# Optimization experiments

Measured on AMD Instinct MI355X. Metric: run time of the kernel, lower is better.

The kernel has to match this reference:

```python
import jax, jax.numpy as jnp
import numpy as np

B, L, D = 4, 1024, 256
HD = 16                 # head_dim
H = D // HD             # num heads = 16
DI = 2 * D              # mamba d_inner (expand=2) = 512
S = 64                  # d_state
KC = 4                  # d_conv
DTR = max(1, D // 16)   # dt_rank = 16
SCALES = (1, 2, 4, 8)


def _lin_interp(x, L_out):
    # F.interpolate(mode='linear', align_corners=False) on (B, L_in, D)
    L_in = x.shape[1]
    pos = (jnp.arange(L_out, dtype=x.dtype) + 0.5) * (L_in / L_out) - 0.5
    pos = jnp.clip(pos, 0.0, L_in - 1)
    lo = jnp.floor(pos).astype(jnp.int32)
    hi = jnp.minimum(lo + 1, L_in - 1)
    w = (pos - lo.astype(x.dtype))[None, :, None]
    return x[:, lo] * (1.0 - w) + x[:, hi] * w


def setup_inputs() -> dict:
    key = jax.random.key(0)
    ks = jax.random.split(key, 24)
    sc = 0.02
    inp = {
        "x": jax.random.normal(ks[0], (B, L, D), jnp.float32),
        "ln_g": jnp.ones((D,), jnp.float32),
        "ln_b": jnp.zeros((D,), jnp.float32),
        # MultiScaleQuery: 4 per-scale projections + fuse
        "mq_w": sc * jax.random.normal(ks[1], (4, D, D), jnp.float32),
        "mq_b": sc * jax.random.normal(ks[2], (4, D), jnp.float32),
        "fuse_w": sc * jax.random.normal(ks[3], (D, 4 * D), jnp.float32),
        "fuse_b": sc * jax.random.normal(ks[4], (D,), jnp.float32),
        # Mamba params
        "in_proj_w": sc * jax.random.normal(ks[5], (2 * DI, D), jnp.float32),
        "conv_w": 0.2 * jax.random.normal(ks[6], (DI, KC), jnp.float32),
        "conv_b": sc * jax.random.normal(ks[7], (DI,), jnp.float32),
        "x_proj_w": sc * jax.random.normal(ks[8], (DTR + 2 * S, DI), jnp.float32),
        "dt_w": sc * jax.random.normal(ks[9], (DI, DTR), jnp.float32),
        "dt_b": jnp.full((DI,), -4.0, jnp.float32),  # softplus -> small dt
        "A_log": jnp.log(jnp.tile(jnp.arange(1, S + 1, dtype=jnp.float32), (DI, 1))),
        "D_ssm": jnp.ones((DI,), jnp.float32),
        "out_w": sc * jax.random.normal(ks[10], (D, DI), jnp.float32),
        # StructuredSSD (q comes from MultiScaleQuery override; q_proj unused)
        "k_w": sc * jax.random.normal(ks[11], (D, D), jnp.float32),
        "k_b": sc * jax.random.normal(ks[12], (D,), jnp.float32),
        "v_w": sc * jax.random.normal(ks[13], (D, D), jnp.float32),
        "v_b": sc * jax.random.normal(ks[14], (D,), jnp.float32),
        "o_w": sc * jax.random.normal(ks[15], (D, D), jnp.float32),
        "o_b": sc * jax.random.normal(ks[16], (D,), jnp.float32),
        "log_tau": jnp.full((H,), np.log(16.0), jnp.float32),
        # Gate
        "gate_w": sc * jax.random.normal(ks[17], (D, 2 * D), jnp.float32),
        "gate_b": sc * jax.random.normal(ks[18], (D,), jnp.float32),
    }
    return inp


def reference(x, ln_g, ln_b, mq_w, mq_b, fuse_w, fuse_b,
              in_proj_w, conv_w, conv_b, x_proj_w, dt_w, dt_b,
              A_log, D_ssm, out_w,
              k_w, k_b, v_w, v_b, o_w, o_b, log_tau,
              gate_w, gate_b):
    Bsz, Lq, Dm = x.shape

    # ---- LayerNorm ----
    mu = x.mean(-1, keepdims=True)
    var = ((x - mu) ** 2).mean(-1, keepdims=True)
    xn = (x - mu) / jnp.sqrt(var + 1e-5) * ln_g + ln_b

    # ---- MultiScaleQuery ----
    qs = []
    for i, s in enumerate(SCALES):
        if s <= 1:
            q = xn @ mq_w[i].T + mq_b[i]
        else:
            xd = xn.reshape(Bsz, Lq // s, s, Dm).mean(2)   # avg_pool1d(k=s, stride=s)
            qd = xd @ mq_w[i].T + mq_b[i]
            q = _lin_interp(qd, Lq)
        qs.append(q)
    q = jnp.concatenate(qs, -1) @ fuse_w.T + fuse_b        # (B, L, D)

    # ---- Mamba (selective scan) ----
    xz = xn @ in_proj_w.T                                  # (B, L, 2*DI)
    xm, z = jnp.split(xz, 2, axis=-1)
    xp = jnp.pad(xm, ((0, 0), (KC - 1, 0), (0, 0)))        # causal depthwise conv
    xc = sum(xp[:, kk:kk + Lq, :] * conv_w[:, kk] for kk in range(KC)) + conv_b
    xc = jax.nn.silu(xc)                                   # (B, L, DI)
    dbc = xc @ x_proj_w.T                                  # (B, L, DTR+2S)
    dt_in, Bm, Cm = jnp.split(dbc, [DTR, DTR + S], axis=-1)
    dt = jax.nn.softplus(dt_in @ dt_w.T + dt_b)            # (B, L, DI)
    A = -jnp.exp(A_log)                                    # (DI, S)

    def step(h, inp):
        xt, dtt, Bt, Ct = inp                              # (B,DI) (B,DI) (B,S) (B,S)
        dA = jnp.exp(dtt[:, :, None] * A)                  # (B, DI, S)
        h = dA * h + (dtt * xt)[:, :, None] * Bt[:, None, :]
        y = jnp.einsum('bds,bs->bd', h, Ct)
        return h, y

    h0 = jnp.zeros((Bsz, DI, S), x.dtype)
    _, ys = jax.lax.scan(step, h0, (xc.transpose(1, 0, 2), dt.transpose(1, 0, 2),
                                    Bm.transpose(1, 0, 2), Cm.transpose(1, 0, 2)))
    y = ys.transpose(1, 0, 2) + xc * D_ssm                 # (B, L, DI)
    y = y * jax.nn.silu(z)
    ssm_out = y @ out_w.T                                  # (B, L, D)

    # ---- StructuredSSD (decay-masked attention, q override) ----
    k = xn @ k_w.T + k_b
    v = xn @ v_w.T + v_b
    hds = lambda t: t.reshape(Bsz, Lq, H, HD).transpose(0, 2, 1, 3)
    qh, kh, vh = hds(q), hds(k), hds(v)                    # (B, H, L, hd)
    scale = 1.0 / np.sqrt(HD)
    scores = jnp.einsum('bhqd,bhkd->bhqk', qh, kh) * scale
    idx = jnp.arange(Lq)
    dist = jnp.maximum(idx[:, None] - idx[None, :], 0).astype(x.dtype)
    tau = jnp.exp(log_tau)[:, None, None]                  # (H,1,1)
    mask = jnp.exp(-dist / tau)                            # (H, L, L); ==1 above diag
    scores = scores * mask
    denom = jnp.maximum(mask.sum(-1, keepdims=True), 1e-6)
    scores = scores / denom                                # broadcast over batch
    attn = jnp.einsum('bhqk,bhkd->bhqd', scores, vh)
    attn = attn.transpose(0, 2, 1, 3).reshape(Bsz, Lq, Dm)
    ssd_out = attn @ o_w.T + o_b

    # ---- Sigmoid gate fusion + residual ----
    gate = jax.nn.sigmoid(jnp.concatenate([ssm_out, ssd_out], -1) @ gate_w.T + gate_b)
    fused = gate * ssm_out + (1.0 - gate) * ssd_out
    return x + fused
```

## Files before the change

### kernel.cpp

```cpp
#include <hip/hip_runtime.h>
#include <math.h>

#define Bsz 4
#define Lseq 1024
#define Dm 256
#define Hh 16
#define HDm 16
#define DIm 512
#define Ssz 64
#define DTRm 16
#define NCH (Bsz * DIm)
#define CHK 64
#define NCHK (Lseq / CHK)
#define CHA 16
#define NCA (Lseq / CHA)
#define LOG2E 1.44269504088896f

typedef __attribute__((ext_vector_type(8))) short s8v;
typedef __attribute__((ext_vector_type(4))) short s4v;
typedef __attribute__((ext_vector_type(4))) float f4v;
typedef unsigned short u16;

static __device__ __forceinline__ float wave_sum(float v) {
    #pragma unroll
    for (int m = 32; m >= 1; m >>= 1) v += __shfl_xor(v, m, 64);
    return v;
}

static __device__ __forceinline__ float bcast(float v, int l) {
    return __uint_as_float(__builtin_amdgcn_readlane(__float_as_uint(v), l));
}

static __device__ __forceinline__ short f2bf(float f) {
    unsigned int u = __float_as_uint(f);
    u = (u + 0x7fffu + ((u >> 16) & 1u)) >> 16;
    return (short)u;
}

static __device__ __forceinline__ float bf2f(u16 u) {
    return __uint_as_float(((unsigned int)u) << 16);
}

static __device__ __forceinline__ s8v pack8(float4 a, float4 b) {
    s8v v;
    v[0] = f2bf(a.x); v[1] = f2bf(a.y); v[2] = f2bf(a.z); v[3] = f2bf(a.w);
    v[4] = f2bf(b.x); v[5] = f2bf(b.y); v[6] = f2bf(b.z); v[7] = f2bf(b.w);
    return v;
}

static __device__ __forceinline__ s4v pack4(float4 a) {
    s4v v;
    v[0] = f2bf(a.x); v[1] = f2bf(a.y); v[2] = f2bf(a.z); v[3] = f2bf(a.w);
    return v;
}

static __device__ __forceinline__ void mfma_core(const u16* __restrict__ A, int lda,
                                                 const u16* __restrict__ W, int ldw,
                                                 int m0, int n0, int K,
                                                 u16 (*As)[40], u16 (*Ws)[40],
                                                 f4v acc[2][2], int tid) {
    int wave = tid >> 6, lane = tid & 63;
    int quad = lane >> 4, r = lane & 15;
    int mo = (wave >> 1) * 32, no = (wave & 1) * 32;
    for (int k0 = 0; k0 < K; k0 += 32) {
        {
            int m = tid >> 2, kk = (tid & 3) * 8;
            *(s8v*)&As[m][kk] = *(const s8v*)(A + (size_t)(m0 + m) * lda + k0 + kk);
        }
        {
            int n = tid >> 2, kk = (tid & 3) * 8;
            *(s8v*)&Ws[n][kk] = *(const s8v*)(W + (size_t)(n0 + n) * ldw + k0 + kk);
        }
        __syncthreads();
        s8v af[2], bf[2];
        #pragma unroll
        for (int i = 0; i < 2; i++) af[i] = *(const s8v*)&As[mo + i * 16 + r][quad * 8];
        #pragma unroll
        for (int j = 0; j < 2; j++) bf[j] = *(const s8v*)&Ws[no + j * 16 + r][quad * 8];
        #pragma unroll
        for (int i = 0; i < 2; i++)
            #pragma unroll
            for (int j = 0; j < 2; j++)
                acc[i][j] = __builtin_amdgcn_mfma_f32_16x16x32_bf16(af[i], bf[j], acc[i][j], 0, 0, 0);
        __syncthreads();
    }
}

#define WB_INPJ 0
#define WB_K    262144
#define WB_V    327680
#define WB_MQ   393216
#define WB_FUSE 655360
#define WB_XP   917504
#define WB_OUT  991232
#define WB_O    1122304
#define WB_GATE 1187840
#define WB_OUTT 1318912
#define WB_WDT  1449984
#define WB_W1P  1712128

__global__ __launch_bounds__(256) void ln_pool(const float* __restrict__ x,
                                               const float* __restrict__ g,
                                               const float* __restrict__ bb,
                                               u16* __restrict__ xnb, u16* __restrict__ xd2b,
                                               u16* __restrict__ xd4b, u16* __restrict__ xd8b,
                                               const float* __restrict__ in_proj_w,
                                               const float* __restrict__ k_w,
                                               const float* __restrict__ v_w,
                                               const float* __restrict__ mq_w,
                                               const float* __restrict__ fuse_w,
                                               const float* __restrict__ x_proj_w,
                                               const float* __restrict__ out_w,
                                               const float* __restrict__ o_w,
                                               const float* __restrict__ gate_w,
                                               const float* __restrict__ dt_w,
                                               u16* __restrict__ wbf) {
    int bx = blockIdx.x;
    int tid = threadIdx.x;
    if (bx < 512) {
        __shared__ float p2[4][256];
        int wid = tid >> 6, lane = tid & 63;
        int gr0 = bx * 8;
        int b = gr0 >> 10, t0 = gr0 & 1023;
        float4 g4 = *(const float4*)(g + lane * 4);
        float4 b4 = *(const float4*)(bb + lane * 4);
        float4 res[2];
        #pragma unroll
        for (int rr = 0; rr < 2; rr++) {
            int row = gr0 + wid * 2 + rr;
            float4 xv = *(const float4*)(x + (size_t)row * 256 + lane * 4);
            float s = wave_sum(xv.x + xv.y + xv.z + xv.w);
            float mean = s * (1.0f / 256.0f);
            float d0 = xv.x - mean, d1 = xv.y - mean, d2 = xv.z - mean, d3 = xv.w - mean;
            float s2 = wave_sum(d0 * d0 + d1 * d1 + d2 * d2 + d3 * d3);
            float inv = rsqrtf(s2 * (1.0f / 256.0f) + 1e-5f);
            float4 r;
            r.x = d0 * inv * g4.x + b4.x; r.y = d1 * inv * g4.y + b4.y;
            r.z = d2 * inv * g4.z + b4.z; r.w = d3 * inv * g4.w + b4.w;
            *(s4v*)(xnb + (size_t)row * 256 + lane * 4) = pack4(r);
            res[rr] = r;
        }
        float4 a2;
        a2.x = 0.5f * (res[0].x + res[1].x); a2.y = 0.5f * (res[0].y + res[1].y);
        a2.z = 0.5f * (res[0].z + res[1].z); a2.w = 0.5f * (res[0].w + res[1].w);
        *(s4v*)(xd2b + (size_t)(b * 512 + (t0 >> 1) + wid) * 256 + lane * 4) = pack4(a2);
        *(float4*)&p2[wid][lane * 4] = a2;
        __syncthreads();
        if (wid < 2) {
            float4 u = *(const float4*)&p2[2 * wid][lane * 4];
            float4 w = *(const float4*)&p2[2 * wid + 1][lane * 4];
            float4 m;
            m.x = 0.5f * (u.x + w.x); m.y = 0.5f * (u.y + w.y);
            m.z = 0.5f * (u.z + w.z); m.w = 0.5f * (u.w + w.w);
            *(s4v*)(xd4b + (size_t)(b * 256 + (t0 >> 2) + wid) * 256 + lane * 4) = pack4(m);
        } else if (wid == 2) {
            float4 q0 = *(const float4*)&p2[0][lane * 4];
            float4 q1 = *(const float4*)&p2[1][lane * 4];
            float4 q2 = *(const float4*)&p2[2][lane * 4];
            float4 q3 = *(const float4*)&p2[3][lane * 4];
            float4 m;
            m.x = 0.25f * ((q0.x + q1.x) + (q2.x + q3.x));
            m.y = 0.25f * ((q0.y + q1.y) + (q2.y + q3.y));
            m.z = 0.25f * ((q0.z + q1.z) + (q2.z + q3.z));
            m.w = 0.25f * ((q0.w + q1.w) + (q2.w + q3.w));
            *(s4v*)(xd8b + (size_t)(b * 128 + (t0 >> 3)) * 256 + lane * 4) = pack4(m);
        }
    } else if (bx < 1156) {
        int l = bx - 512;
        const float* src; u16* dst; int base;
        if (l < 128)      { src = in_proj_w; dst = wbf + WB_INPJ; base = l; }
        else if (l < 160) { src = k_w;      dst = wbf + WB_K;    base = l - 128; }
        else if (l < 192) { src = v_w;      dst = wbf + WB_V;    base = l - 160; }
        else if (l < 320) { src = mq_w;     dst = wbf + WB_MQ;   base = l - 192; }
        else if (l < 448) { src = fuse_w;   dst = wbf + WB_FUSE; base = l - 320; }
        else if (l < 484) { src = x_proj_w; dst = wbf + WB_XP;   base = l - 448; }
        else if (l < 548) { src = out_w;    dst = wbf + WB_OUT;  base = l - 484; }
        else if (l < 580) { src = o_w;      dst = wbf + WB_O;    base = l - 548; }
        else              { src = gate_w;   dst = wbf + WB_GATE; base = l - 580; }
        int idx = base * 2048 + tid * 8;
        const float* sp = src + idx;
        *(s8v*)(dst + idx) = pack8(*(const float4*)sp, *(const float4*)(sp + 4));
    } else if (bx < 1412) {
        int l = bx - 1156;
        int gid = l * 1024 + tid * 4;
        int n = gid >> 9, d0 = gid & 511;
        float4 acc = {0.f, 0.f, 0.f, 0.f};
        #pragma unroll
        for (int k = 0; k < 16; k++) {
            float wv = dt_w[n * 16 + k];
            float4 xp = *(const float4*)(x_proj_w + (size_t)k * 512 + d0);
            acc.x = fmaf(wv, xp.x, acc.x); acc.y = fmaf(wv, xp.y, acc.y);
            acc.z = fmaf(wv, xp.z, acc.z); acc.w = fmaf(wv, xp.w, acc.w);
        }
        *(s4v*)(wbf + WB_WDT + (size_t)n * 512 + d0) = pack4(acc);
    } else {
        int l = bx - 1412;
        int gid = l * 2048 + tid * 8;
        int k = gid >> 9, d0 = gid & 511;
        float4 a0 = *(const float4*)(out_w + (size_t)k * 512 + d0);
        float4 a1 = *(const float4*)(out_w + (size_t)k * 512 + d0 + 4);
        float vv[8] = {a0.x, a0.y, a0.z, a0.w, a1.x, a1.y, a1.z, a1.w};
        #pragma unroll
        for (int i = 0; i < 8; i++)
            wbf[WB_OUTT + (size_t)(d0 + i) * 256 + k] = (u16)f2bf(vv[i]);
    }
}

__global__ __launch_bounds__(256) void proj8(const u16* __restrict__ xnb,
                                             const u16* __restrict__ xd2b,
                                             const u16* __restrict__ xd4b,
                                             const u16* __restrict__ xd8b,
                                             u16* __restrict__ wbf,
                                             const float* __restrict__ k_b,
                                             const float* __restrict__ v_b,
                                             const float* __restrict__ mq_b,
                                             u16* __restrict__ xmb, float* __restrict__ zT,
                                             float* __restrict__ kmat, float* __restrict__ vmat,
                                             u16* __restrict__ q0b, u16* __restrict__ qd2b,
                                             u16* __restrict__ qd4b, u16* __restrict__ qd8b) {
    __shared__ u16 As[64][40];
    __shared__ u16 Ws[64][40];
    int bx = blockIdx.x;
    int tid = threadIdx.x;
    const u16* A; const u16* W; const float* bias;
    float* Cf = nullptr; u16* Cb = nullptr;
    int lda, ldw, ldc, K = 256, n0, m0;
    if (bx < 512) {
        A = xnb; lda = 256; W = wbf + WB_INPJ; ldw = 256; bias = nullptr; Cb = xmb; ldc = DIm;
        n0 = (bx & 7) * 64; m0 = (bx >> 3) * 64;
    } else if (bx < 1024) {
        int l = bx - 512;
        A = wbf + WB_INPJ + 131072; lda = 256; W = xnb; ldw = 256; bias = nullptr;
        Cf = zT; ldc = 4096;
        m0 = (l >> 6) * 64; n0 = (l & 63) * 64;
    } else if (bx < 1280) {
        int l = bx - 1024;
        A = xnb; lda = 256; W = wbf + WB_K; ldw = 256; bias = k_b; Cf = kmat; ldc = Dm;
        n0 = (l & 3) * 64; m0 = (l >> 2) * 64;
    } else if (bx < 1536) {
        int l = bx - 1280;
        A = xnb; lda = 256; W = wbf + WB_V; ldw = 256; bias = v_b; Cf = vmat; ldc = Dm;
        n0 = (l & 3) * 64; m0 = (l >> 2) * 64;
    } else if (bx < 1792) {
        int l = bx - 1536;
        A = xnb; lda = 256; W = wbf + WB_MQ; ldw = 256; bias = mq_b; Cb = q0b; ldc = Dm;
        n0 = (l & 3) * 64; m0 = (l >> 2) * 64;
    } else if (bx < 1920) {
        int l = bx - 1792;
        A = xd2b; lda = 256; W = wbf + WB_MQ + 65536; ldw = 256; bias = mq_b + 256; Cb = qd2b; ldc = Dm;
        n0 = (l & 3) * 64; m0 = (l >> 2) * 64;
    } else if (bx < 1984) {
        int l = bx - 1920;
        A = xd4b; lda = 256; W = wbf + WB_MQ + 131072; ldw = 256; bias = mq_b + 512; Cb = qd4b; ldc = Dm;
        n0 = (l & 3) * 64; m0 = (l >> 2) * 64;
    } else {
        if (bx < 2016) {
            int l = bx - 1984;
            A = xd8b; lda = 256; W = wbf + WB_MQ + 196608; ldw = 256; bias = mq_b + 768; Cb = qd8b; ldc = Dm;
            n0 = (l & 3) * 64; m0 = (l >> 2) * 64;
        } else {
            int l = bx - 2016;
            A = wbf + WB_GATE; lda = 512; W = wbf + WB_OUTT; ldw = 256; bias = nullptr;
            Cb = wbf + WB_W1P; ldc = 512;
            m0 = (l >> 3) * 64; n0 = (l & 7) * 64;
        }
    }
    f4v acc[2][2];
    #pragma unroll
    for (int i = 0; i < 2; i++)
        #pragma unroll
        for (int j = 0; j < 2; j++) acc[i][j] = (f4v){0.f, 0.f, 0.f, 0.f};
    mfma_core(A, lda, W, ldw, m0, n0, K, As, Ws, acc, tid);
    int wave = tid >> 6, lane = tid & 63;
    int quad = lane >> 4, r = lane & 15;
    int mo = (wave >> 1) * 32, no = (wave & 1) * 32;
    #pragma unroll
    for (int i = 0; i < 2; i++)
        #pragma unroll
        for (int j = 0; j < 2; j++)
            #pragma unroll
            for (int reg = 0; reg < 4; reg++) {
                int m = m0 + mo + i * 16 + quad * 4 + reg;
                int n = n0 + no + j * 16 + r;
                float v = acc[i][j][reg];
                if (bias) v += bias[n];
                if (Cb) Cb[(size_t)m * ldc + n] = (u16)f2bf(v);
                else Cf[(size_t)m * ldc + n] = v;
            }
}

__global__ __launch_bounds__(256) void mid2(const u16* __restrict__ q0b,
                                            const u16* __restrict__ qd2b,
                                            const u16* __restrict__ qd4b,
                                            const u16* __restrict__ qd8b,
                                            const u16* __restrict__ w_fuse,
                                            const float* __restrict__ fuse_b,
                                            float* __restrict__ qbuf,
                                            const u16* __restrict__ xmb,
                                            const float* __restrict__ cw,
                                            const float* __restrict__ cb,
                                            u16* __restrict__ xcb, float* __restrict__ xcT) {
    __shared__ __align__(16) char smem[16640];
    int bx = blockIdx.x;
    int tid = threadIdx.x;
    if (bx < 256) {
        u16 (*As)[40] = (u16(*)[40])smem;
        u16 (*Ws)[40] = (u16(*)[40])(smem + 5120);
        int wave = tid >> 6, lane = tid & 63;
        int quad = lane >> 4, r = lane & 15;
        int n0 = (bx & 3) * 64, m0 = (bx >> 2) * 64;
        int mo = (wave >> 1) * 32, no = (wave & 1) * 32;
        f4v acc[2][2];
        #pragma unroll
        for (int i = 0; i < 2; i++)
            #pragma unroll
            for (int j = 0; j < 2; j++) acc[i][j] = (f4v){0.f, 0.f, 0.f, 0.f};
        for (int k0 = 0; k0 < 1024; k0 += 32) {
            {
                int m = tid >> 2, kk = (tid & 3) * 8;
                int kg = k0 + kk;
                int seg = kg >> 8, dcol = kg & 255;
                int mg = m0 + m;
                s8v pv;
                if (seg == 0) {
                    pv = *(const s8v*)(q0b + (size_t)mg * 256 + dcol);
                } else {
                    int t = mg & 1023, b = mg >> 10;
                    int Lin = 512 >> (seg - 1);
                    const u16* qd = (seg == 1) ? qd2b : (seg == 2) ? qd4b : qd8b;
                    float pos = (t + 0.5f) * ((float)Lin / 1024.0f) - 0.5f;
                    pos = fminf(fmaxf(pos, 0.0f), (float)(Lin - 1));
                    int lo = (int)floorf(pos);
                    int hi = min(lo + 1, Lin - 1);
                    float w = pos - (float)lo;
                    s8v lv = *(const s8v*)(qd + ((size_t)(b * Lin + lo)) * 256 + dcol);
                    s8v hv = *(const s8v*)(qd + ((size_t)(b * Lin + hi)) * 256 + dcol);
                    #pragma unroll
                    for (int i = 0; i < 8; i++) {
                        float lf = bf2f((u16)lv[i]), hf = bf2f((u16)hv[i]);
                        pv[i] = f2bf(lf + w * (hf - lf));
                    }
                }
                *(s8v*)&As[m][kk] = pv;
            }
            {
                int n = tid >> 2, kk = (tid & 3) * 8;
                *(s8v*)&Ws[n][kk] = *(const s8v*)(w_fuse + (size_t)(n0 + n) * 1024 + k0 + kk);
            }
            __syncthreads();
            s8v af[2], bf[2];
            #pragma unroll
            for (int i = 0; i < 2; i++) af[i] = *(const s8v*)&As[mo + i * 16 + r][quad * 8];
            #pragma unroll
            for (int j = 0; j < 2; j++) bf[j] = *(const s8v*)&Ws[no + j * 16 + r][quad * 8];
            #pragma unroll
            for (int i = 0; i < 2; i++)
                #pragma unroll
                for (int j = 0; j < 2; j++)
                    acc[i][j] = __builtin_amdgcn_mfma_f32_16x16x32_bf16(af[i], bf[j], acc[i][j], 0, 0, 0);
            __syncthreads();
        }
        #pragma unroll
        for (int i = 0; i < 2; i++)
            #pragma unroll
            for (int j = 0; j < 2; j++)
                #pragma unroll
                for (int reg = 0; reg < 4; reg++) {
                    int m = m0 + mo + i * 16 + quad * 4 + reg;
                    int n = n0 + no + j * 16 + r;
                    qbuf[(size_t)m * 256 + n] = acc[i][j][reg] + fuse_b[n];
                }
    } else {
        float (*tile)[65] = (float(*)[65])smem;
        int blk = bx - 256;
        int cblk = blk & 7;
        int tblk = (blk >> 3) & 15;
        int b = blk >> 7;
        int c0 = cblk * 64, t0 = tblk * 64;
        int cc = tid & 63;
        int tw = tid >> 6;
        int c = c0 + cc;
        float w0 = cw[c * 4 + 0], w1 = cw[c * 4 + 1], w2 = cw[c * 4 + 2], w3 = cw[c * 4 + 3];
        float bias = cb[c];
        #pragma unroll 4
        for (int i = 0; i < 16; i++) {
            int tl = tw * 16 + i;
            int t = t0 + tl;
            const u16* base = xmb + ((size_t)(b * Lseq + t)) * DIm + c;
            float acc = bias + bf2f(base[0]) * w3;
            if (t >= 3) {
                acc += bf2f(base[-3 * DIm]) * w0 + bf2f(base[-2 * DIm]) * w1 + bf2f(base[-1 * DIm]) * w2;
            } else {
                if (t >= 1) acc += bf2f(base[-1 * DIm]) * w2;
                if (t >= 2) acc += bf2f(base[-2 * DIm]) * w1;
            }
            float r = acc / (1.0f + __expf(-acc));
            xcb[((size_t)(b * Lseq + t)) * DIm + c] = (u16)f2bf(r);
            tile[tl][cc] = r;
        }
        __syncthreads();
        int tcol = tid & 63;
        int crow0 = tid >> 6;
        #pragma unroll 4
        for (int j = 0; j < 16; j++) {
            int crow = crow0 * 16 + j;
            xcT[((size_t)(c0 + crow)) * (Bsz * Lseq) + b * Lseq + t0 + tcol] = tile[tcol][crow];
        }
    }
}

__global__ __launch_bounds__(256) void xproj_ap1(const u16* __restrict__ xcb,
                                                 const u16* __restrict__ wbf,
                                                 float* __restrict__ dbc2,
                                                 const float* __restrict__ dt_b,
                                                 float* __restrict__ dtmT,
                                                 const float* __restrict__ kmat,
                                                 const float* __restrict__ vmat,
                                                 const float* __restrict__ log_tau,
                                                 float* __restrict__ loc) {
    __shared__ __align__(16) char smem[10240];
    int bx = blockIdx.x;
    int tid = threadIdx.x;
    int wid = tid >> 6, lane = tid & 63;
    if (bx < 640) {
        u16 (*As)[40] = (u16(*)[40])smem;
        u16 (*Ws)[40] = (u16(*)[40])(smem + 5120);
        const u16* A; const u16* W;
        int lda, ldw, K, m0, n0, mode;
        if (bx < 128) {
            A = xcb; lda = 512; W = wbf + WB_XP + 16 * 512; ldw = 512; K = 512;
            n0 = (bx & 1) * 64; m0 = (bx >> 1) * 64; mode = 0;
        } else {
            int l = bx - 128;
            A = wbf + WB_WDT; lda = 512; W = xcb; ldw = 512; K = 512;
            m0 = (l >> 6) * 64; n0 = (l & 63) * 64; mode = 1;
        }
        f4v acc[2][2];
        #pragma unroll
        for (int i = 0; i < 2; i++)
            #pragma unroll
            for (int j = 0; j < 2; j++) acc[i][j] = (f4v){0.f, 0.f, 0.f, 0.f};
        mfma_core(A, lda, W, ldw, m0, n0, K, As, Ws, acc, tid);
        int quad = lane >> 4, r = lane & 15;
        int mo = (wid >> 1) * 32, no = (wid & 1) * 32;
        #pragma unroll
        for (int i = 0; i < 2; i++)
            #pragma unroll
            for (int j = 0; j < 2; j++)
                #pragma unroll
                for (int reg = 0; reg < 4; reg++) {
                    int m = m0 + mo + i * 16 + quad * 4 + reg;
                    int n = n0 + no + j * 16 + r;
                    float v = acc[i][j][reg];
                    if (mode == 0) {
                        dbc2[(size_t)m * 128 + n] = v;
                    } else {
                        v += dt_b[m];
                        v = fmaxf(v, 0.0f) + log1pf(__expf(-fabsf(v)));
                        dtmT[(size_t)m * 4096 + n] = v;
                    }
                }
    } else {
        float (*Ksh)[CHA][20] = (float(*)[CHA][20])smem;
        float (*Vsh)[CHA][16] = (float(*)[CHA][16])(smem + 5120);
        int wv = (bx - 640) * 4 + wid;
        int bh = wv >> 6, c = wv & 63;
        int b = bh >> 4, h = bh & 15;
        float inv_tau = __expf(-log_tau[h]);
        float rdec = __expf(-inv_tau);
        int t0 = c * CHA;
        int row = lane >> 2, q4 = (lane & 3) * 4;
        const float* kp = kmat + ((size_t)(b * Lseq + t0 + row)) * Dm + h * HDm + q4;
        const float* vp = vmat + ((size_t)(b * Lseq + t0 + row)) * Dm + h * HDm + q4;
        *(float4*)&Ksh[wid][row][q4] = *(const float4*)kp;
        *(float4*)&Vsh[wid][row][q4] = *(const float4*)vp;
        int g = lane >> 4, cc = lane & 15;
        float4 U = {0.f, 0.f, 0.f, 0.f}, T = {0.f, 0.f, 0.f, 0.f};
        #pragma unroll
        for (int s = 0; s < CHA; s++) {
            float4 kf = *(const float4*)&Ksh[wid][s][4 * g];
            float vv = Vsh[wid][s][cc];
            float u0 = kf.x * vv, u1 = kf.y * vv, u2 = kf.z * vv, u3 = kf.w * vv;
            U.x += u0; U.y += u1; U.z += u2; U.w += u3;
            T.x = fmaf(rdec, T.x, u0); T.y = fmaf(rdec, T.y, u1);
            T.z = fmaf(rdec, T.z, u2); T.w = fmaf(rdec, T.w, u3);
        }
        float* op = loc + ((size_t)bh * NCA + c) * 512;
        *(float4*)(op + lane * 4) = U;
        *(float4*)(op + 256 + lane * 4) = T;
    }
}

__global__ __launch_bounds__(256) void sp1_ap2(const float* __restrict__ xcT,
                                               const float* __restrict__ dtmT,
                                               const float* __restrict__ dbc2,
                                               const float* __restrict__ A_log,
                                               float* __restrict__ hloc,
                                               float* __restrict__ Pc,
                                               float* __restrict__ loc,
                                               const float* __restrict__ log_tau,
                                               float* __restrict__ kvtot) {
    int bx = blockIdx.x;
    int tid = threadIdx.x;
    int wid = tid >> 6, lane = tid & 63;
    if (bx < 8192) {
        int wave = bx * 4 + wid;
        int ch = wave & (NCH - 1);
        int c  = wave >> 11;
        int b = ch >> 9, d = ch & (DIm - 1);
        float As2 = -__expf(A_log[d * Ssz + lane]) * LOG2E;
        int base_m = b * Lseq + c * CHK;
        float dt_vec = dtmT[(size_t)d * (Bsz * Lseq) + base_m + lane];
        float x_vec  = xcT [(size_t)d * (Bsz * Lseq) + base_m + lane];
        float ux = dt_vec * x_vec;
        float S = dt_vec;
        #pragma unroll
        for (int m = 1; m < 64; m <<= 1) {
            float o = __shfl_up(S, m, 64);
            if (lane >= m) S += o;
        }
        float Stot = bcast(S, 63);
        const float* Bp = dbc2 + (size_t)base_m * 128 + lane;
        float h0 = 0.f, h1 = 0.f, h2 = 0.f, h3 = 0.f;
        #pragma unroll 4
        for (int t = 0; t < CHK; t += 4) {
            float B0 = Bp[0], B1 = Bp[128], B2 = Bp[256], B3 = Bp[384];
            Bp += 512;
            float w0 = exp2f(As2 * (Stot - bcast(S, t)))     * bcast(ux, t);
            float w1 = exp2f(As2 * (Stot - bcast(S, t + 1))) * bcast(ux, t + 1);
            float w2 = exp2f(As2 * (Stot - bcast(S, t + 2))) * bcast(ux, t + 2);
            float w3 = exp2f(As2 * (Stot - bcast(S, t + 3))) * bcast(ux, t + 3);
            h0 = fmaf(w0, B0, h0); h1 = fmaf(w1, B1, h1);
            h2 = fmaf(w2, B2, h2); h3 = fmaf(w3, B3, h3);
        }
        size_t o = ((size_t)ch * NCHK + c) * Ssz + lane;
        hloc[o] = (h0 + h1) + (h2 + h3);
        Pc[o] = exp2f(As2 * Stot);
    } else {
        int bh = bx - 8192, e = tid;
        float inv_tau = __expf(-log_tau[bh & 15]);
        float rp = __expf(-(float)CHA * inv_tau);
        float* lp = loc + (size_t)bh * NCA * 512;
        float Ua = 0.f, Ta = 0.f;
        #pragma unroll 8
        for (int c = 0; c < NCA; c++) {
            float tu = lp[c * 512 + e];
            lp[c * 512 + e] = Ua;
            Ua += tu;
            float tt = lp[c * 512 + 256 + e];
            lp[c * 512 + 256 + e] = Ta;
            Ta = fmaf(rp, Ta, tt);
        }
        kvtot[bh * 256 + e] = Ua;
    }
}

__global__ __launch_bounds__(256) void comb_ap3(float* __restrict__ hloc,
                                                const float* __restrict__ Pc,
                                                const float* __restrict__ q,
                                                const float* __restrict__ kmat,
                                                const float* __restrict__ vmat,
                                                const float* __restrict__ log_tau,
                                                const float* __restrict__ init,
                                                const float* __restrict__ kvtot,
                                                u16* __restrict__ attnb) {
    __shared__ __align__(16) char smem[18432];
    int bx = blockIdx.x;
    int tid = threadIdx.x;
    int wid = tid >> 6, lane = tid & 63;
    if (bx < 512) {
        int wave = bx * 4 + wid;
        size_t base = (size_t)wave * NCHK * Ssz + lane;
        float H = 0.0f;
        #pragma unroll
        for (int c = 0; c < NCHK; c++) {
            size_t o = base + (size_t)c * Ssz;
            float p = Pc[o];
            float hl = hloc[o];
            hloc[o] = H;
            H = fmaf(p, H, hl);
        }
    } else {
        float (*Ksh)[CHA][20] = (float(*)[CHA][20])smem;
        float (*Qsh)[CHA][20] = (float(*)[CHA][20])(smem + 5120);
        float (*Vsh)[CHA][16] = (float(*)[CHA][16])(smem + 10240);
        float (*Ysh)[CHA][16] = (float(*)[CHA][16])(smem + 14336);
        int wv = (bx - 512) * 4 + wid;
        int bh = wv >> 6, c = wv & 63;
        int b = bh >> 4, h = bh & 15;
        float inv_tau = __expf(-log_tau[h]);
        float rdec = __expf(-inv_tau);
        int t0 = c * CHA;
        int row = lane >> 2, q4 = (lane & 3) * 4;
        const float* kp = kmat + ((size_t)(b * Lseq + t0 + row)) * Dm + h * HDm + q4;
        const float* vp = vmat + ((size_t)(b * Lseq + t0 + row)) * Dm + h * HDm + q4;
        const float* qp = q    + ((size_t)(b * Lseq + t0 + row)) * Dm + h * HDm + q4;
        *(float4*)&Ksh[wid][row][q4] = *(const float4*)kp;
        *(float4*)&Vsh[wid][row][q4] = *(const float4*)vp;
        *(float4*)&Qsh[wid][row][q4] = *(const float4*)qp;
        int g = lane >> 4, cc = lane & 15;
        size_t ibase = ((size_t)bh * NCA + c) * 512;
        float4 U  = *(const float4*)(init + ibase + lane * 4);
        float4 T  = *(const float4*)(init + ibase + 256 + lane * 4);
        float4 KV = *(const float4*)(kvtot + bh * 256 + lane * 4);
        float om = 1.0f - rdec;
        float geom = (om > 1e-8f) ? (1.0f - __expf(-inv_tau * (float)t0)) / om : (float)t0;
        #pragma unroll
        for (int s = 0; s < CHA; s++) {
            int i = t0 + s;
            geom = fmaf(geom, rdec, 1.0f);
            float4 kf = *(const float4*)&Ksh[wid][s][4 * g];
            float4 qf = *(const float4*)&Qsh[wid][s][4 * g];
            float vv = Vsh[wid][s][cc];
            float u0 = kf.x * vv, u1 = kf.y * vv, u2 = kf.z * vv, u3 = kf.w * vv;
            U.x += u0; U.y += u1; U.z += u2; U.w += u3;
            T.x = fmaf(rdec, T.x, u0); T.y = fmaf(rdec, T.y, u1);
            T.z = fmaf(rdec, T.z, u2); T.w = fmaf(rdec, T.w, u3);
            float p;
            p = qf.x * (KV.x - U.x + T.x);
            p = fmaf(qf.y, KV.y - U.y + T.y, p);
            p = fmaf(qf.z, KV.z - U.z + T.z, p);
            p = fmaf(qf.w, KV.w - U.w + T.w, p);
            p += __shfl_xor(p, 16, 64);
            p += __shfl_xor(p, 32, 64);
            float deno = fmaxf((float)(Lseq - 1 - i) + geom, 1e-6f);
            float yv = p * (0.25f / deno);
            if (lane < 16) Ysh[wid][s][lane] = yv;
        }
        float4 yv4 = *(const float4*)&Ysh[wid][row][q4];
        *(s4v*)(attnb + ((size_t)(b * Lseq + t0 + row)) * Dm + h * HDm + q4) = pack4(yv4);
    }
}

__global__ __launch_bounds__(256) void p3_og(const float* __restrict__ xcT,
                                             const float* __restrict__ dtmT,
                                             const float* __restrict__ zT,
                                             const float* __restrict__ dbc2,
                                             const float* __restrict__ A_log,
                                             const float* __restrict__ D_ssm,
                                             const float* __restrict__ Hinit,
                                             u16* __restrict__ yTb,
                                             const u16* __restrict__ attnb,
                                             const u16* __restrict__ w_o,
                                             const float* __restrict__ o_b,
                                             u16* __restrict__ cat2b) {
    __shared__ __align__(16) char smem[17408];
    int bx = blockIdx.x;
    int tid = threadIdx.x;
    int wid = tid >> 6, lane = tid & 63;
    if (bx < 8192) {
        float (*hCs)[16][68] = (float(*)[16][68])smem;
        int wave = bx * 4 + wid;
        int ch = wave & (NCH - 1);
        int c  = wave >> 11;
        int b = ch >> 9, d = ch & (DIm - 1);
        float As2 = -__expf(A_log[d * Ssz + lane]) * LOG2E;
        float Dd = D_ssm[d];
        int base_m = b * Lseq + c * CHK;
        float dt_vec = dtmT[(size_t)d * (Bsz * Lseq) + base_m + lane];
        float x_vec  = xcT [(size_t)d * (Bsz * Lseq) + base_m + lane];
        float zown   = zT  [(size_t)d * (Bsz * Lseq) + base_m + lane];
        float ux = dt_vec * x_vec;
        const float* Bp = dbc2 + (size_t)base_m * 128 + lane;
        const float* Cp = Bp + 64;
        float h = Hinit[((size_t)ch * NCHK + c) * Ssz + lane];
        float yred = 0.0f;
        int tl = lane >> 2;
        int so = (lane & 3) * 16;
        for (int tb = 0; tb < 4; tb++) {
            #pragma unroll
            for (int j = 0; j < 16; j++) {
                int t = tb * 16 + j;
                float Bt = *Bp; Bp += 128;
                float Ct = *Cp; Cp += 128;
                float dtv = bcast(dt_vec, t);
                float u   = bcast(ux, t);
                float dA = exp2f(As2 * dtv);
                h = fmaf(dA, h, u * Bt);
                hCs[wid][j][lane] = h * Ct;
            }
            const float* bp = &hCs[wid][tl][so];
            float4 a0 = *(const float4*)(bp + 0);
            float4 a1 = *(const float4*)(bp + 4);
            float4 a2 = *(const float4*)(bp + 8);
            float4 a3 = *(const float4*)(bp + 12);
            float part = ((a0.x + a0.y) + (a0.z + a0.w)) + ((a1.x + a1.y) + (a1.z + a1.w))
                       + ((a2.x + a2.y) + (a2.z + a2.w)) + ((a3.x + a3.y) + (a3.z + a3.w));
            part += __shfl_xor(part, 1, 64);
            part += __shfl_xor(part, 2, 64);
            float got = __shfl(part, ((lane - tb * 16) << 2) & 63, 64);
            if ((lane >> 4) == tb) yred = got;
        }
        float yg = (yred + x_vec * Dd) * (zown / (1.0f + __expf(-zown)));
        yTb[(size_t)d * (Bsz * Lseq) + base_m + lane] = (u16)f2bf(yg);
    } else {
        u16 (*As)[40] = (u16(*)[40])smem;
        u16 (*Ws)[40] = (u16(*)[40])(smem + 5120);
        int l = bx - 8192;
        int n0 = (l & 3) * 64, m0 = (l >> 2) * 64;
        f4v acc[2][2];
        #pragma unroll
        for (int i = 0; i < 2; i++)
            #pragma unroll
            for (int j = 0; j < 2; j++) acc[i][j] = (f4v){0.f, 0.f, 0.f, 0.f};
        mfma_core(attnb, 256, w_o, 256, m0, n0, 256, As, Ws, acc, tid);
        int quad = lane >> 4, r = lane & 15;
        int mo = (wid >> 1) * 32, no = (wid & 1) * 32;
        #pragma unroll
        for (int i = 0; i < 2; i++)
            #pragma unroll
            for (int j = 0; j < 2; j++)
                #pragma unroll
                for (int reg = 0; reg < 4; reg++) {
                    int m = m0 + mo + i * 16 + quad * 4 + reg;
                    int n = n0 + no + j * 16 + r;
                    cat2b[(size_t)m * 512 + 256 + n] = (u16)f2bf(acc[i][j][reg] + o_b[n]);
                }
    }
}

__global__ __launch_bounds__(256) void outg_gpre(const u16* __restrict__ yTb,
                                                 const u16* __restrict__ wbf,
                                                 const u16* __restrict__ cat2b_ssd,
                                                 u16* __restrict__ cat2b,
                                                 float* __restrict__ gpre1,
                                                 float* __restrict__ gpre2) {
    __shared__ u16 As[64][40];
    __shared__ u16 Ws[64][40];
    int bx = blockIdx.x;
    int tid = threadIdx.x;
    int wave = tid >> 6, lane = tid & 63;
    int quad = lane >> 4, r = lane & 15;
    int mo = (wave >> 1) * 32, no = (wave & 1) * 32;
    f4v acc[2][2];
    #pragma unroll
    for (int i = 0; i < 2; i++)
        #pragma unroll
        for (int j = 0; j < 2; j++) acc[i][j] = (f4v){0.f, 0.f, 0.f, 0.f};
    if (bx < 512) {
        int mode = bx >> 8;
        int l = bx & 255;
        int n0 = (l & 3) * 64, m0 = (l >> 2) * 64;
        const u16* W = mode ? (wbf + WB_W1P) : (wbf + WB_OUT);
        for (int k0 = 0; k0 < 512; k0 += 32) {
            {
                int k = tid >> 3, m8 = (tid & 7) * 8;
                s8v av = *(const s8v*)(yTb + (size_t)(k0 + k) * (Bsz * Lseq) + m0 + m8);
                #pragma unroll
                for (int i = 0; i < 8; i++) As[m8 + i][k] = (u16)av[i];
            }
            {
                int n = tid >> 2, kk = (tid & 3) * 8;
                *(s8v*)&Ws[n][kk] = *(const s8v*)(W + (size_t)(n0 + n) * 512 + k0 + kk);
            }
            __syncthreads();
            s8v af[2], bf[2];
            #pragma unroll
            for (int i = 0; i < 2; i++) af[i] = *(const s8v*)&As[mo + i * 16 + r][quad * 8];
            #pragma unroll
            for (int j = 0; j < 2; j++) bf[j] = *(const s8v*)&Ws[no + j * 16 + r][quad * 8];
            #pragma unroll
            for (int i = 0; i < 2; i++)
                #pragma unroll
                for (int j = 0; j < 2; j++)
                    acc[i][j] = __builtin_amdgcn_mfma_f32_16x16x32_bf16(af[i], bf[j], acc[i][j], 0, 0, 0);
            __syncthreads();
        }
        #pragma unroll
        for (int i = 0; i < 2; i++)
            #pragma unroll
            for (int j = 0; j < 2; j++)
                #pragma unroll
                for (int reg = 0; reg < 4; reg++) {
                    int m = m0 + mo + i * 16 + quad * 4 + reg;
                    int n = n0 + no + j * 16 + r;
                    if (mode) gpre1[(size_t)m * 256 + n] = acc[i][j][reg];
                    else cat2b[(size_t)m * 512 + n] = (u16)f2bf(acc[i][j][reg]);
                }
    } else {
        int l = bx - 512;
        int n0 = (l & 3) * 64, m0 = (l >> 2) * 64;
        mfma_core(cat2b_ssd, 512, wbf + WB_GATE + 256, 512, m0, n0, 256, As, Ws, acc, tid);
        #pragma unroll
        for (int i = 0; i < 2; i++)
            #pragma unroll
            for (int j = 0; j < 2; j++)
                #pragma unroll
                for (int reg = 0; reg < 4; reg++) {
                    int m = m0 + mo + i * 16 + quad * 4 + reg;
                    int n = n0 + no + j * 16 + r;
                    gpre2[(size_t)m * 256 + n] = acc[i][j][reg];
                }
    }
}

__global__ __launch_bounds__(256) void final_k(const float* __restrict__ gpre1,
                                               const float* __restrict__ gpre2,
                                               const float* __restrict__ gate_b,
                                               const u16* __restrict__ cat2b,
                                               const float* __restrict__ x,
                                               float* __restrict__ outp) {
    int idx4 = (blockIdx.x * 256 + threadIdx.x) * 4;
    int m = idx4 >> 8, n = idx4 & 255;
    float4 g1 = *(const float4*)(gpre1 + (size_t)m * 256 + n);
    float4 g2 = *(const float4*)(gpre2 + (size_t)m * 256 + n);
    float4 gb = *(const float4*)(gate_b + n);
    s4v sm = *(const s4v*)(cat2b + (size_t)m * 512 + n);
    s4v sd = *(const s4v*)(cat2b + (size_t)m * 512 + 256 + n);
    float4 xv = *(const float4*)(x + (size_t)m * 256 + n);
    float4 o;
    float gv[4] = {g1.x + g2.x + gb.x, g1.y + g2.y + gb.y,
                   g1.z + g2.z + gb.z, g1.w + g2.w + gb.w};
    float xr[4] = {xv.x, xv.y, xv.z, xv.w};
    float* op = (float*)&o;
    #pragma unroll
    for (int i = 0; i < 4; i++) {
        float gg = 1.0f / (1.0f + __expf(-gv[i]));
        float ssm = bf2f((u16)sm[i]);
        float ssd = bf2f((u16)sd[i]);
        op[i] = xr[i] + gg * ssm + (1.0f - gg) * ssd;
    }
    *(float4*)(outp + (size_t)m * 256 + n) = o;
}

extern "C" void kernel_launch(void* const* d_in, const int* in_sizes, int n_in,
                              void* d_out, int out_size, void* d_ws, size_t ws_size,
                              hipStream_t stream) {
    const float* x        = (const float*)d_in[0];
    const float* ln_g     = (const float*)d_in[1];
    const float* ln_b     = (const float*)d_in[2];
    const float* mq_w     = (const float*)d_in[3];
    const float* mq_b     = (const float*)d_in[4];
    const float* fuse_w   = (const float*)d_in[5];
    const float* fuse_b   = (const float*)d_in[6];
    const float* in_proj_w= (const float*)d_in[7];
    const float* conv_w   = (const float*)d_in[8];
    const float* conv_b   = (const float*)d_in[9];
    const float* x_proj_w = (const float*)d_in[10];
    const float* dt_w     = (const float*)d_in[11];
    const float* dt_b     = (const float*)d_in[12];
    const float* A_log    = (const float*)d_in[13];
    const float* D_ssm    = (const float*)d_in[14];
    const float* out_w    = (const float*)d_in[15];
    const float* k_w      = (const float*)d_in[16];
    const float* k_b      = (const float*)d_in[17];
    const float* v_w      = (const float*)d_in[18];
    const float* v_b      = (const float*)d_in[19];
    const float* o_w      = (const float*)d_in[20];
    const float* o_b      = (const float*)d_in[21];
    const float* log_tau  = (const float*)d_in[22];
    const float* gate_w   = (const float*)d_in[23];
    const float* gate_b   = (const float*)d_in[24];
    float* outp = (float*)d_out;

    const int M = Bsz * Lseq;
    float* ws = (float*)d_ws;
    size_t off = 0;
    float* zT    = ws + off; off += (size_t)DIm * M;
    float* xcT   = ws + off; off += (size_t)DIm * M;
    float* dtmT  = ws + off; off += (size_t)DIm * M;
    float* dbc2  = ws + off; off += (size_t)M * 128;
    float* qbuf  = ws + off; off += (size_t)M * Dm;
    float* kmat  = ws + off; off += (size_t)M * Dm;
    float* vmat  = ws + off; off += (size_t)M * Dm;
    float* loc   = ws + off; off += (size_t)64 * NCA * 512;
    float* hloc  = ws + off; off += (size_t)NCH * NCHK * Ssz;
    float* Pc    = ws + off; off += (size_t)NCH * NCHK * Ssz;
    float* kvtot = ws + off; off += (size_t)64 * 256;
    float* gpre1 = ws + off; off += (size_t)M * Dm;
    float* gpre2 = ws + off; off += (size_t)M * Dm;
    u16* ub = (u16*)(ws + off);
    size_t uo = 0;
    u16* xnb  = ub + uo; uo += (size_t)M * Dm;
    u16* xmb  = ub + uo; uo += (size_t)M * DIm;
    u16* xd2b = ub + uo; uo += (size_t)2048 * Dm;
    u16* xd4b = ub + uo; uo += (size_t)1024 * Dm;
    u16* xd8b = ub + uo; uo += (size_t)512 * Dm;
    u16* q0b  = ub + uo; uo += (size_t)M * Dm;
    u16* qd2b = ub + uo; uo += (size_t)2048 * Dm;
    u16* qd4b = ub + uo; uo += (size_t)1024 * Dm;
    u16* qd8b = ub + uo; uo += (size_t)512 * Dm;
    u16* attnb= ub + uo; uo += (size_t)M * Dm;
    u16* cat2b= ub + uo; uo += (size_t)M * 2 * Dm;
    u16* yTb  = ub + uo; uo += (size_t)DIm * M;
    u16* wbf  = ub + uo; uo += 1843200;
    u16* xcb  = cat2b;

    ln_pool<<<1476, 256, 0, stream>>>(x, ln_g, ln_b, xnb, xd2b, xd4b, xd8b,
        in_proj_w, k_w, v_w, mq_w, fuse_w, x_proj_w, out_w, o_w, gate_w, dt_w, wbf);

    proj8<<<2048, 256, 0, stream>>>(xnb, xd2b, xd4b, xd8b, wbf,
        k_b, v_b, mq_b, xmb, zT, kmat, vmat, q0b, qd2b, qd4b, qd8b);

    mid2<<<768, 256, 0, stream>>>(q0b, qd2b, qd4b, qd8b, wbf + WB_FUSE, fuse_b, qbuf,
        xmb, conv_w, conv_b, xcb, xcT);

    xproj_ap1<<<1664, 256, 0, stream>>>(xcb, wbf, dbc2, dt_b, dtmT, kmat, vmat, log_tau, loc);

    sp1_ap2<<<8256, 256, 0, stream>>>(xcT, dtmT, dbc2, A_log, hloc, Pc, loc, log_tau, kvtot);

    comb_ap3<<<1536, 256, 0, stream>>>(hloc, Pc, qbuf, kmat, vmat, log_tau, loc, kvtot, attnb);

    p3_og<<<8448, 256, 0, stream>>>(xcT, dtmT, zT, dbc2, A_log, D_ssm, hloc, yTb,
        attnb, wbf + WB_O, o_b, cat2b);

    outg_gpre<<<768, 256, 0, stream>>>(yTb, wbf, cat2b + 256, cat2b, gpre1, gpre2);

    final_k<<<1024, 256, 0, stream>>>(gpre1, gpre2, gate_b, cat2b, x, outp);
}
```

Measured before the change: 316.8 us.

## Fold o_proj into gate pre-activation weights to drop a dependent GEMM stage

Precomputes W2P = gate_w[:,256:] @ o_w and c2 = gate_w[:,256:] @ o_b during setup, so the SSD half of the gate pre-activation is computed straight from attn instead of from the o_proj output. This removes the data dependency between o_proj and the gate GEMM, letting o_proj, out_proj, and both gate GEMMs run in one launch (big4). The SSD o_proj GEMM moves out of the scan kernel, which is now a pure scan. It adds weight-prep work and changes bf16 rounding slightly, because the folded weights are rounded once instead of the intermediate activation.

Measured after the change: 326.0 us. 2.9% more time.

```diff
diff --git a/kernel.cpp b/kernel.cpp
--- a/kernel.cpp
+++ b/kernel.cpp
@@ -98,6 +98,8 @@
 #define WB_OUTT 1318912
 #define WB_WDT  1449984
 #define WB_W1P  1712128
+#define WB_OT   1843200
+#define WB_W2P  1908736
 
 __global__ __launch_bounds__(256) void ln_pool(const float* __restrict__ x,
                                                const float* __restrict__ g,
@@ -114,7 +116,9 @@
                                                const float* __restrict__ o_w,
                                                const float* __restrict__ gate_w,
                                                const float* __restrict__ dt_w,
-                                               u16* __restrict__ wbf) {
+                                               const float* __restrict__ o_b,
+                                               u16* __restrict__ wbf,
+                                               float* __restrict__ c2) {
     int bx = blockIdx.x;
     int tid = threadIdx.x;
     if (bx < 512) {
@@ -193,7 +197,7 @@
             acc.z = fmaf(wv, xp.z, acc.z); acc.w = fmaf(wv, xp.w, acc.w);
         }
         *(s4v*)(wbf + WB_WDT + (size_t)n * 512 + d0) = pack4(acc);
-    } else {
+    } else if (bx < 1476) {
         int l = bx - 1412;
         int gid = l * 2048 + tid * 8;
         int k = gid >> 9, d0 = gid & 511;
@@ -203,6 +207,21 @@
         #pragma unroll
         for (int i = 0; i < 8; i++)
             wbf[WB_OUTT + (size_t)(d0 + i) * 256 + k] = (u16)f2bf(vv[i]);
+    } else if (bx < 1508) {
+        int l = bx - 1476;
+        int gid = l * 2048 + tid * 8;
+        int d = gid >> 8, k0 = gid & 255;
+        float4 a0 = *(const float4*)(o_w + (size_t)d * 256 + k0);
+        float4 a1 = *(const float4*)(o_w + (size_t)d * 256 + k0 + 4);
+        float vv[8] = {a0.x, a0.y, a0.z, a0.w, a1.x, a1.y, a1.z, a1.w};
+        #pragma unroll
+        for (int i = 0; i < 8; i++)
+            wbf[WB_OT + (size_t)(k0 + i) * 256 + d] = (u16)f2bf(vv[i]);
+    } else {
+        float s = 0.0f;
+        const float* gw = gate_w + (size_t)tid * 512 + 256;
+        for (int d = 0; d < 256; d++) s = fmaf(gw[d], o_b[d], s);
+        c2[tid] = s;
     }
 }
 
@@ -253,17 +272,20 @@
         int l = bx - 1920;
         A = xd4b; lda = 256; W = wbf + WB_MQ + 131072; ldw = 256; bias = mq_b + 512; Cb = qd4b; ldc = Dm;
         n0 = (l & 3) * 64; m0 = (l >> 2) * 64;
+    } else if (bx < 2016) {
+        int l = bx - 1984;
+        A = xd8b; lda = 256; W = wbf + WB_MQ + 196608; ldw = 256; bias = mq_b + 768; Cb = qd8b; ldc = Dm;
+        n0 = (l & 3) * 64; m0 = (l >> 2) * 64;
+    } else if (bx < 2048) {
+        int l = bx - 2016;
+        A = wbf + WB_GATE; lda = 512; W = wbf + WB_OUTT; ldw = 256; bias = nullptr;
+        Cb = wbf + WB_W1P; ldc = 512;
+        m0 = (l >> 3) * 64; n0 = (l & 7) * 64;
     } else {
-        if (bx < 2016) {
-            int l = bx - 1984;
-            A = xd8b; lda = 256; W = wbf + WB_MQ + 196608; ldw = 256; bias = mq_b + 768; Cb = qd8b; ldc = Dm;
-            n0 = (l & 3) * 64; m0 = (l >> 2) * 64;
-        } else {
-            int l = bx - 2016;
-            A = wbf + WB_GATE; lda = 512; W = wbf + WB_OUTT; ldw = 256; bias = nullptr;
-            Cb = wbf + WB_W1P; ldc = 512;
-            m0 = (l >> 3) * 64; n0 = (l & 7) * 64;
-        }
+        int l = bx - 2048;
+        A = wbf + WB_GATE + 256; lda = 512; W = wbf + WB_OT; ldw = 256; bias = nullptr;
+        Cb = wbf + WB_W2P; ldc = 256;
+        m0 = (l >> 2) * 64; n0 = (l & 3) * 64;
     }
     f4v acc[2][2];
     #pragma unroll
@@ -632,103 +654,77 @@
     }
 }
 
-__global__ __launch_bounds__(256) void p3_og(const float* __restrict__ xcT,
-                                             const float* __restrict__ dtmT,
-                                             const float* __restrict__ zT,
-                                             const float* __restrict__ dbc2,
-                                             const float* __restrict__ A_log,
-                                             const float* __restrict__ D_ssm,
-                                             const float* __restrict__ Hinit,
-                                             u16* __restrict__ yTb,
-                                             const u16* __restrict__ attnb,
-                                             const u16* __restrict__ w_o,
-                                             const float* __restrict__ o_b,
-                                             u16* __restrict__ cat2b) {
-    __shared__ __align__(16) char smem[17408];
-    int bx = blockIdx.x;
-    int tid = threadIdx.x;
-    int wid = tid >> 6, lane = tid & 63;
-    if (bx < 8192) {
-        float (*hCs)[16][68] = (float(*)[16][68])smem;
-        int wave = bx * 4 + wid;
-        int ch = wave & (NCH - 1);
-        int c  = wave >> 11;
-        int b = ch >> 9, d = ch & (DIm - 1);
-        float As2 = -__expf(A_log[d * Ssz + lane]) * LOG2E;
-        float Dd = D_ssm[d];
-        int base_m = b * Lseq + c * CHK;
-        float dt_vec = dtmT[(size_t)d * (Bsz * Lseq) + base_m + lane];
-        float x_vec  = xcT [(size_t)d * (Bsz * Lseq) + base_m + lane];
-        float zown   = zT  [(size_t)d * (Bsz * Lseq) + base_m + lane];
-        float ux = dt_vec * x_vec;
-        const float* Bp = dbc2 + (size_t)base_m * 128 + lane;
-        const float* Cp = Bp + 64;
-        float h = Hinit[((size_t)ch * NCHK + c) * Ssz + lane];
-        float yred = 0.0f;
-        int tl = lane >> 2;
-        int so = (lane & 3) * 16;
-        for (int tb = 0; tb < 4; tb++) {
-            #pragma unroll
-            for (int j = 0; j < 16; j++) {
-                int t = tb * 16 + j;
-                float Bt = *Bp; Bp += 128;
-                float Ct = *Cp; Cp += 128;
-                float dtv = bcast(dt_vec, t);
-                float u   = bcast(ux, t);
-                float dA = exp2f(As2 * dtv);
-                h = fmaf(dA, h, u * Bt);
-                hCs[wid][j][lane] = h * Ct;
-            }
-            const float* bp = &hCs[wid][tl][so];
-            float4 a0 = *(const float4*)(bp + 0);
-            float4 a1 = *(const float4*)(bp + 4);
-            float4 a2 = *(const float4*)(bp + 8);
-            float4 a3 = *(const float4*)(bp + 12);
-            float part = ((a0.x + a0.y) + (a0.z + a0.w)) + ((a1.x + a1.y) + (a1.z + a1.w))
-                       + ((a2.x + a2.y) + (a2.z + a2.w)) + ((a3.x + a3.y) + (a3.z + a3.w));
-            part += __shfl_xor(part, 1, 64);
-            part += __shfl_xor(part, 2, 64);
-            float got = __shfl(part, ((lane - tb * 16) << 2) & 63, 64);
-            if ((lane >> 4) == tb) yred = got;
-        }
-        float yg = (yred + x_vec * Dd) * (zown / (1.0f + __expf(-zown)));
-        yTb[(size_t)d * (Bsz * Lseq) + base_m + lane] = (u16)f2bf(yg);
-    } else {
-        u16 (*As)[40] = (u16(*)[40])smem;
-        u16 (*Ws)[40] = (u16(*)[40])(smem + 5120);
-        int l = bx - 8192;
-        int n0 = (l & 3) * 64, m0 = (l >> 2) * 64;
-        f4v acc[2][2];
-        #pragma unroll
-        for (int i = 0; i < 2; i++)
-            #pragma unroll
-            for (int j = 0; j < 2; j++) acc[i][j] = (f4v){0.f, 0.f, 0.f, 0.f};
-        mfma_core(attnb, 256, w_o, 256, m0, n0, 256, As, Ws, acc, tid);
-        int quad = lane >> 4, r = lane & 15;
-        int mo = (wid >> 1) * 32, no = (wid & 1) * 32;
-        #pragma unroll
-        for (int i = 0; i < 2; i++)
-            #pragma unroll
-            for (int j = 0; j < 2; j++)
-                #pragma unroll
-                for (int reg = 0; reg < 4; reg++) {
-                    int m = m0 + mo + i * 16 + quad * 4 + reg;
-                    int n = n0 + no + j * 16 + r;
-                    cat2b[(size_t)m * 512 + 256 + n] = (u16)f2bf(acc[i][j][reg] + o_b[n]);
-                }
+__global__ __launch_bounds__(256) void scan_pass3(const float* __restrict__ xcT,
+                                                  const float* __restrict__ dtmT,
+                                                  const float* __restrict__ zT,
+                                                  const float* __restrict__ dbc2,
+                                                  const float* __restrict__ A_log,
+                                                  const float* __restrict__ D_ssm,
+                                                  const float* __restrict__ Hinit,
+                                                  u16* __restrict__ yTb) {
+    __shared__ float hCs[4][16][68];
+    int wid = threadIdx.x >> 6;
+    int lane = threadIdx.x & 63;
+    int wave = blockIdx.x * 4 + wid;
+    int ch = wave & (NCH - 1);
+    int c  = wave >> 11;
+    int b = ch >> 9, d = ch & (DIm - 1);
+    float As2 = -__expf(A_log[d * Ssz + lane]) * LOG2E;
+    float Dd = D_ssm[d];
+    int base_m = b * Lseq + c * CHK;
+    float dt_vec = dtmT[(size_t)d * (Bsz * Lseq) + base_m + lane];
+    float x_vec  = xcT [(size_t)d * (Bsz * Lseq) + base_m + lane];
+    float zown   = zT  [(size_t)d * (Bsz * Lseq) + base_m + lane];
+    float ux = dt_vec * x_vec;
+    const float* Bp = dbc2 + (size_t)base_m * 128 + lane;
+    const float* Cp = Bp + 64;
+    float h = Hinit[((size_t)ch * NCHK + c) * Ssz + lane];
+    float yred = 0.0f;
+    int tl = lane >> 2;
+    int so = (lane & 3) * 16;
+    for (int tb = 0; tb < 4; tb++) {
+        #pragma unroll
+        for (int j = 0; j < 16; j++) {
+            int t = tb * 16 + j;
+            float Bt = *Bp; Bp += 128;
+            float Ct = *Cp; Cp += 128;
+            float dtv = bcast(dt_vec, t);
+            float u   = bcast(ux, t);
+            float dA = exp2f(As2 * dtv);
+            h = fmaf(dA, h, u * Bt);
+            hCs[wid][j][lane] = h * Ct;
+        }
+        const float* bp = &hCs[wid][tl][so];
+        float4 a0 = *(const float4*)(bp + 0);
+        float4 a1 = *(const float4*)(bp + 4);
+        float4 a2 = *(const float4*)(bp + 8);
+        float4 a3 = *(const float4*)(bp + 12);
+        float part = ((a0.x + a0.y) + (a0.z + a0.w)) + ((a1.x + a1.y) + (a1.z + a1.w))
+                   + ((a2.x + a2.y) + (a2.z + a2.w)) + ((a3.x + a3.y) + (a3.z + a3.w));
+        part += __shfl_xor(part, 1, 64);
+        part += __shfl_xor(part, 2, 64);
+        float got = __shfl(part, ((lane - tb * 16) << 2) & 63, 64);
+        if ((lane >> 4) == tb) yred = got;
     }
-}
-
-__global__ __launch_bounds__(256) void outg_gpre(const u16* __restrict__ yTb,
-                                                 const u16* __restrict__ wbf,
-                                                 const u16* __restrict__ cat2b_ssd,
-                                                 u16* __restrict__ cat2b,
-                                                 float* __restrict__ gpre1,
-                                                 float* __restrict__ gpre2) {
+    float yg = (yred + x_vec * Dd) * (zown / (1.0f + __expf(-zown)));
+    yTb[(size_t)d * (Bsz * Lseq) + base_m + lane] = (u16)f2bf(yg);
+}
+
+__global__ __launch_bounds__(256) void big4(const u16* __restrict__ attnb,
+                                            const u16* __restrict__ yTb,
+                                            const u16* __restrict__ wbf,
+                                            const float* __restrict__ o_b,
+                                            const float* __restrict__ c2,
+                                            u16* __restrict__ cat2b,
+                                            float* __restrict__ gpre1,
+                                            float* __restrict__ gpre2) {
     __shared__ u16 As[64][40];
     __shared__ u16 Ws[64][40];
     int bx = blockIdx.x;
     int tid = threadIdx.x;
+    int mode = bx >> 8;
+    int l = bx & 255;
+    int n0 = (l & 3) * 64, m0 = (l >> 2) * 64;
     int wave = tid >> 6, lane = tid & 63;
     int quad = lane >> 4, r = lane & 15;
     int mo = (wave >> 1) * 32, no = (wave & 1) * 32;
@@ -737,11 +733,24 @@
     for (int i = 0; i < 2; i++)
         #pragma unroll
         for (int j = 0; j < 2; j++) acc[i][j] = (f4v){0.f, 0.f, 0.f, 0.f};
-    if (bx < 512) {
-        int mode = bx >> 8;
-        int l = bx & 255;
-        int n0 = (l & 3) * 64, m0 = (l >> 2) * 64;
-        const u16* W = mode ? (wbf + WB_W1P) : (wbf + WB_OUT);
+    if (mode == 0 || mode == 3) {
+        const u16* W = (mode == 0) ? (wbf + WB_O) : (wbf + WB_W2P);
+        mfma_core(attnb, 256, W, 256, m0, n0, 256, As, Ws, acc, tid);
+        #pragma unroll
+        for (int i = 0; i < 2; i++)
+            #pragma unroll
+            for (int j = 0; j < 2; j++)
+                #pragma unroll
+                for (int reg = 0; reg < 4; reg++) {
+                    int m = m0 + mo + i * 16 + quad * 4 + reg;
+                    int n = n0 + no + j * 16 + r;
+                    if (mode == 0)
+                        cat2b[(size_t)m * 512 + 256 + n] = (u16)f2bf(acc[i][j][reg] + o_b[n]);
+                    else
+                        gpre2[(size_t)m * 256 + n] = acc[i][j][reg] + c2[n];
+                }
+    } else {
+        const u16* W = (mode == 1) ? (wbf + WB_OUT) : (wbf + WB_W1P);
         for (int k0 = 0; k0 < 512; k0 += 32) {
             {
                 int k = tid >> 3, m8 = (tid & 7) * 8;
@@ -774,22 +783,8 @@
                 for (int reg = 0; reg < 4; reg++) {
                     int m = m0 + mo + i * 16 + quad * 4 + reg;
                     int n = n0 + no + j * 16 + r;
-                    if (mode) gpre1[(size_t)m * 256 + n] = acc[i][j][reg];
-                    else cat2b[(size_t)m * 512 + n] = (u16)f2bf(acc[i][j][reg]);
-                }
-    } else {
-        int l = bx - 512;
-        int n0 = (l & 3) * 64, m0 = (l >> 2) * 64;
-        mfma_core(cat2b_ssd, 512, wbf + WB_GATE + 256, 512, m0, n0, 256, As, Ws, acc, tid);
-        #pragma unroll
-        for (int i = 0; i < 2; i++)
-            #pragma unroll
-            for (int j = 0; j < 2; j++)
-                #pragma unroll
-                for (int reg = 0; reg < 4; reg++) {
-                    int m = m0 + mo + i * 16 + quad * 4 + reg;
-                    int n = n0 + no + j * 16 + r;
-                    gpre2[(size_t)m * 256 + n] = acc[i][j][reg];
+                    if (mode == 1) cat2b[(size_t)m * 512 + n] = (u16)f2bf(acc[i][j][reg]);
+                    else gpre1[(size_t)m * 256 + n] = acc[i][j][reg];
                 }
     }
 }
@@ -869,6 +864,7 @@
     float* kvtot = ws + off; off += (size_t)64 * 256;
     float* gpre1 = ws + off; off += (size_t)M * Dm;
     float* gpre2 = ws + off; off += (size_t)M * Dm;
+    float* c2    = ws + off; off += 256;
     u16* ub = (u16*)(ws + off);
     size_t uo = 0;
     u16* xnb  = ub + uo; uo += (size_t)M * Dm;
@@ -883,13 +879,13 @@
     u16* attnb= ub + uo; uo += (size_t)M * Dm;
     u16* cat2b= ub + uo; uo += (size_t)M * 2 * Dm;
     u16* yTb  = ub + uo; uo += (size_t)DIm * M;
-    u16* wbf  = ub + uo; uo += 1843200;
+    u16* wbf  = ub + uo; uo += 1974272;
     u16* xcb  = cat2b;
 
-    ln_pool<<<1476, 256, 0, stream>>>(x, ln_g, ln_b, xnb, xd2b, xd4b, xd8b,
-        in_proj_w, k_w, v_w, mq_w, fuse_w, x_proj_w, out_w, o_w, gate_w, dt_w, wbf);
-
-    proj8<<<2048, 256, 0, stream>>>(xnb, xd2b, xd4b, xd8b, wbf,
+    ln_pool<<<1509, 256, 0, stream>>>(x, ln_g, ln_b, xnb, xd2b, xd4b, xd8b,
+        in_proj_w, k_w, v_w, mq_w, fuse_w, x_proj_w, out_w, o_w, gate_w, dt_w, o_b, wbf, c2);
+
+    proj8<<<2064, 256, 0, stream>>>(xnb, xd2b, xd4b, xd8b, wbf,
         k_b, v_b, mq_b, xmb, zT, kmat, vmat, q0b, qd2b, qd4b, qd8b);
 
     mid2<<<768, 256, 0, stream>>>(q0b, qd2b, qd4b, qd8b, wbf + WB_FUSE, fuse_b, qbuf,
@@ -901,10 +897,9 @@
 
     comb_ap3<<<1536, 256, 0, stream>>>(hloc, Pc, qbuf, kmat, vmat, log_tau, loc, kvtot, attnb);
 
-    p3_og<<<8448, 256, 0, stream>>>(xcT, dtmT, zT, dbc2, A_log, D_ssm, hloc, yTb,
-        attnb, wbf + WB_O, o_b, cat2b);
-
-    outg_gpre<<<768, 256, 0, stream>>>(yTb, wbf, cat2b + 256, cat2b, gpre1, gpre2);
+    scan_pass3<<<8192, 256, 0, stream>>>(xcT, dtmT, zT, dbc2, A_log, D_ssm, hloc, yTb);
+
+    big4<<<1024, 256, 0, stream>>>(attnb, yTb, wbf, o_b, c2, cat2b, gpre1, gpre2);
 
     final_k<<<1024, 256, 0, stream>>>(gpre1, gpre2, gate_b, cat2b, x, outp);
 }
```
